# Kernel tuning notes

Hardware: AMD Instinct MI355X
Metric: run time of the kernel (lower is better)

## Reference

```python
import jax, jax.numpy as jnp
import numpy as np

N = 50000       # nodes
E = 800000      # directed edges (before self-loops)
D_IN = 128
H = 32          # hidden width, heads=1 (PyG SuperGATConv defaults)
D_OUT = 16
L = 15          # stacked SuperGATConv layers
NEG_SLOPE = 0.2


def setup_inputs() -> dict:
    key = jax.random.key(0)
    ks = jax.random.split(key, 8)
    s_in = 1.0 / np.sqrt(D_IN)
    s_h = 1.0 / np.sqrt(H)
    return dict(
        x=jax.random.normal(ks[0], (N, D_IN), jnp.float32),
        edge_index=jax.random.randint(ks[1], (2, E), 0, N, jnp.int32),
        W0=jax.random.normal(ks[2], (D_IN, H), jnp.float32) * s_in,
        b0=jnp.zeros((H,), jnp.float32),
        Ws=jax.random.normal(ks[3], (L, H, H), jnp.float32) * s_h,
        att_l=jax.random.normal(ks[4], (L, H), jnp.float32) * s_h,
        att_r=jax.random.normal(ks[5], (L, H), jnp.float32) * s_h,
        bs=jnp.zeros((L, H), jnp.float32),
        W16=jax.random.normal(ks[6], (H, D_OUT), jnp.float32) * s_h,
        b16=jnp.zeros((D_OUT,), jnp.float32),
    )


def _supergat(h, src, dst, W, al, ar, b):
    # One SuperGATConv (attention_type='MX', heads=1, concat) forward.
    hp = h @ W                          # [N, H] transformed features
    hj = hp[src]                        # [E', H] source (message) features
    hi = hp[dst]                        # [E', H] destination features
    logits = jnp.sum(hi * hj, axis=-1)  # MX dot-product logits
    alpha = hj @ al + hi @ ar           # GAT-style additive scores
    alpha = alpha * jax.nn.sigmoid(logits)
    alpha = jnp.where(alpha >= 0, alpha, NEG_SLOPE * alpha)  # leaky_relu
    # segment softmax over destination nodes
    amax = jax.ops.segment_max(alpha, dst, num_segments=N)
    ex = jnp.exp(alpha - amax[dst])
    den = jax.ops.segment_sum(ex, dst, num_segments=N)
    coef = ex / den[dst]
    out = jax.ops.segment_sum(hj * coef[:, None], dst, num_segments=N)
    return out + b


def reference(x, edge_index, W0, b0, Ws, att_l, att_r, bs, W16, b16):
    # PyG SuperGATConv adds self-loops by default
    loops = jnp.arange(N, dtype=edge_index.dtype)
    src = jnp.concatenate([edge_index[0], loops])
    dst = jnp.concatenate([edge_index[1], loops])
    h = x @ W0 + b0                     # conv0: Linear(in, 32)

    def step(h, p):
        W, al, ar, b = p
        return jax.nn.relu(_supergat(h, src, dst, W, al, ar, b)), None

    h, _ = jax.lax.scan(step, h, (Ws, att_l, att_r, bs))
    return h @ W16 + b16                # conv16: Linear(32, out)
```

## Files before the change

### kernel.cpp

```cpp
#include <hip/hip_runtime.h>
#include <hip/hip_fp16.h>
#include <cmath>
#include <cstring>

#define NN 50000
#define EE 800000
#define ET 850000
#define PADCAP 1004544
#define NBK 831
#define EBINS 196
#define DB 512
#define NB 50

__global__ void k_fill(int* __restrict__ p){
  int i = blockIdx.x*256 + threadIdx.x;
  p[i] = NN;
}

__global__ void k_permfill(int* __restrict__ perm){
  int i = blockIdx.x*256 + threadIdx.x;
  perm[i] = NN;
}

__global__ __launch_bounds__(1024) void k_ebhist(const int* __restrict__ ei,
                                                 int* __restrict__ ebh){
  __shared__ int hist[EBINS];
  int t = threadIdx.x, b = blockIdx.x;
  if (t < EBINS) hist[t] = 0;
  __syncthreads();
  int e = b*1024 + t;
  if (e < ET){
    int d = (e < EE) ? ei[EE + e] : (e - EE);
    atomicAdd(&hist[d >> 8], 1);
  }
  __syncthreads();
  if (t < EBINS) ebh[t*NBK + b] = hist[t];
}

__global__ __launch_bounds__(1024) void k_escan1(const int* __restrict__ ebh,
                                                 int* __restrict__ ebhoff,
                                                 int* __restrict__ btot){
  __shared__ int tmp[1024];
  int bin = blockIdx.x, t = threadIdx.x;
  int v = (t < NBK) ? ebh[bin*NBK + t] : 0;
  int inc = v;
  for (int off = 1; off < 1024; off <<= 1){
    tmp[t] = inc; __syncthreads();
    int add = (t >= off) ? tmp[t - off] : 0;
    __syncthreads();
    inc += add;
  }
  if (t < NBK) ebhoff[bin*NBK + t] = inc - v;
  if (t == 1023) btot[bin] = inc;
}

__global__ __launch_bounds__(256) void k_escan2(const int* __restrict__ btot,
                                                int* __restrict__ bbase){
  __shared__ int tmp[256];
  int t = threadIdx.x;
  int v = (t < EBINS) ? btot[t] : 0;
  int inc = v;
  for (int off = 1; off < 256; off <<= 1){
    tmp[t] = inc; __syncthreads();
    int add = (t >= off) ? tmp[t - off] : 0;
    __syncthreads();
    inc += add;
  }
  if (t < EBINS) bbase[t] = inc - v;
  if (t == 255) bbase[EBINS] = inc;
}

__global__ __launch_bounds__(1024) void k_ebin(const int* __restrict__ ei,
                                               const int* __restrict__ ebhoff,
                                               const int* __restrict__ bbase,
                                               int2* __restrict__ ebuf){
  __shared__ int hist[EBINS];
  int t = threadIdx.x, b = blockIdx.x;
  if (t < EBINS) hist[t] = 0;
  __syncthreads();
  int e = b*1024 + t;
  if (e < ET){
    int s, d;
    if (e < EE){ s = ei[e]; d = ei[EE + e]; } else { s = d = e - EE; }
    int bin = d >> 8;
    int rank = atomicAdd(&hist[bin], 1);
    int pos = bbase[bin] + ebhoff[bin*NBK + b] + rank;
    ebuf[pos] = make_int2(s, d);
  }
}

__global__ __launch_bounds__(1024) void k_ecnt(const int2* __restrict__ ebuf,
                                               const int* __restrict__ bbase,
                                               int* __restrict__ count){
  __shared__ int cnt[256];
  int t = threadIdx.x, bin = blockIdx.x;
  if (t < 256) cnt[t] = 0;
  __syncthreads();
  int rb = bbase[bin], re = bbase[bin+1];
  for (int i = rb + t; i < re; i += 1024) atomicAdd(&cnt[ebuf[i].y - (bin << 8)], 1);
  __syncthreads();
  int idx = (bin << 8) + t;
  if (t < 256 && idx < NN) count[idx] = cnt[t];
}

__global__ void k_bsum(const int* __restrict__ count, int* __restrict__ bsums){
  int i = blockIdx.x*256 + threadIdx.x;
  int v = (i < NN) ? ((count[i] + 3) & ~3) : 0;
  #pragma unroll
  for (int m = 1; m < 64; m <<= 1) v += __shfl_xor(v, m);
  __shared__ int ws[4];
  if ((threadIdx.x & 63) == 0) ws[threadIdx.x >> 6] = v;
  __syncthreads();
  if (threadIdx.x == 0) bsums[blockIdx.x] = ws[0] + ws[1] + ws[2] + ws[3];
}

__global__ void k_bscan(const int* __restrict__ bsums, int* __restrict__ boffs, int nb){
  __shared__ int tmp[256];
  int t = threadIdx.x;
  int self = (t < nb) ? bsums[t] : 0;
  int v = self;
  for (int off = 1; off < 256; off <<= 1){
    tmp[t] = v; __syncthreads();
    int add = (t >= off) ? tmp[t - off] : 0;
    __syncthreads();
    v += add;
  }
  if (t < nb) boffs[t] = v - self;
}

__global__ void k_scan(const int* __restrict__ count, const int* __restrict__ boffs,
                       int* __restrict__ offs){
  __shared__ int tmp[256];
  int t = threadIdx.x;
  int gid = blockIdx.x*256 + t;
  int self = (gid < NN) ? ((count[gid] + 3) & ~3) : 0;
  int v = self;
  for (int off = 1; off < 256; off <<= 1){
    tmp[t] = v; __syncthreads();
    int add = (t >= off) ? tmp[t - off] : 0;
    __syncthreads();
    v += add;
  }
  int excl = v - self + boffs[blockIdx.x];
  if (gid < NN) offs[gid] = excl;
  if (gid == NN-1) offs[NN] = excl + self;
}

__global__ __launch_bounds__(1024) void k_escatter(const int2* __restrict__ ebuf,
                                                   const int* __restrict__ bbase,
                                                   const int* __restrict__ offs,
                                                   int* __restrict__ srcCSR){
  __shared__ int cur[256];
  int t = threadIdx.x, bin = blockIdx.x;
  if (t < 256){ int idx = (bin << 8) + t; cur[t] = (idx < NN) ? offs[idx] : 0; }
  __syncthreads();
  int rb = bbase[bin], re = bbase[bin+1];
  for (int i = rb + t; i < re; i += 1024){
    int2 e = ebuf[i];
    int p = atomicAdd(&cur[e.y - (bin << 8)], 1);
    srcCSR[p] = e.x;
  }
}

__global__ __launch_bounds__(1024) void k_dhist_blk(const int* __restrict__ count,
                                                    int* __restrict__ blockhist){
  __shared__ int hist[DB];
  int t = threadIdx.x, b = blockIdx.x;
  if (t < DB) hist[t] = 0;
  __syncthreads();
  int i = b*1024 + t;
  if (i < NN){
    int deg = count[i]; if (deg > DB-1) deg = DB-1;
    atomicAdd(&hist[DB-1-deg], 1);
  }
  __syncthreads();
  if (t < DB) blockhist[t*NB + b] = hist[t];
}

__global__ __launch_bounds__(DB) void k_dcol(const int* __restrict__ blockhist,
                                             int* __restrict__ blockoffs,
                                             int* __restrict__ dbase){
  int k = threadIdx.x;
  int run = 0;
  #pragma unroll 5
  for (int b = 0; b < NB; ++b){
    int v = blockhist[k*NB + b];
    blockoffs[k*NB + b] = run;
    run += v;
  }
  __shared__ int tmp[DB];
  int v = run;
  for (int off = 1; off < DB; off <<= 1){
    tmp[k] = v; __syncthreads();
    int add = (k >= off) ? tmp[k - off] : 0;
    __syncthreads();
    v += add;
  }
  dbase[k] = v - run;
}

__global__ __launch_bounds__(1024) void k_dscatter_blk(const int* __restrict__ count,
                                                       const int* __restrict__ blockoffs,
                                                       const int* __restrict__ dbase,
                                                       int* __restrict__ perm){
  __shared__ int hist[DB];
  int t = threadIdx.x, b = blockIdx.x;
  if (t < DB) hist[t] = 0;
  __syncthreads();
  int i = b*1024 + t;
  if (i < NN){
    int deg = count[i]; if (deg > DB-1) deg = DB-1;
    int bin = DB-1-deg;
    int rank = atomicAdd(&hist[bin], 1);
    int pos = dbase[bin] + blockoffs[bin*NB + b] + rank;
    perm[pos] = i;
  }
}

__device__ __forceinline__ void cvt8(uint4 r, float* v){
  __half2 h;
  memcpy(&h, &r.x, 4); float2 f = __half22float2(h); v[0]=f.x; v[1]=f.y;
  memcpy(&h, &r.y, 4); f = __half22float2(h); v[2]=f.x; v[3]=f.y;
  memcpy(&h, &r.z, 4); f = __half22float2(h); v[4]=f.x; v[5]=f.y;
  memcpy(&h, &r.w, 4); f = __half22float2(h); v[6]=f.x; v[7]=f.y;
}
__device__ __forceinline__ unsigned pack_h2(float x, float y){
  __half2 h = __floats2half2_rn(x, y);
  unsigned u; memcpy(&u, &h, 4); return u;
}

__global__ __launch_bounds__(256) void k_prologue(
    const float* __restrict__ x, const float* __restrict__ W0, const float* __restrict__ b0,
    const float* __restrict__ Ws0, const float* __restrict__ al0, const float* __restrict__ ar0,
    __half* __restrict__ hp_out, float* __restrict__ hl_out, float* __restrict__ hr_out){
  __shared__ __align__(16) float w0[128*32];
  __shared__ __align__(16) float w1[32*32];
  int t = threadIdx.x;
  for (int i = t; i < 4096; i += 256) w0[i] = W0[i];
  for (int i = t; i < 1024; i += 256) w1[i] = Ws0[i];
  __syncthreads();
  int g = t >> 5, lane = t & 31;
  float bl = b0[lane], alv = al0[lane], arv = ar0[lane];
  #pragma unroll
  for (int p = 0; p < 2; ++p){
    int na = blockIdx.x*32 + p*16 + g;
    int nb = na + 8;
    int nac = (na < NN) ? na : NN-1;
    int nbc = (nb < NN) ? nb : NN-1;
    const float4* xa = (const float4*)(x + (size_t)nac*128);
    const float4* xb4 = (const float4*)(x + (size_t)nbc*128);
    float ha = bl, hb = bl;
    #pragma unroll
    for (int j4 = 0; j4 < 32; ++j4){
      float4 va = xa[j4], vb = xb4[j4];
      float c0 = w0[(j4*4+0)*32 + lane], c1 = w0[(j4*4+1)*32 + lane];
      float c2 = w0[(j4*4+2)*32 + lane], c3 = w0[(j4*4+3)*32 + lane];
      ha += va.x*c0 + va.y*c1 + va.z*c2 + va.w*c3;
      hb += vb.x*c0 + vb.y*c1 + vb.z*c2 + vb.w*c3;
    }
    float hpa = 0.f, hpb = 0.f;
    #pragma unroll
    for (int j = 0; j < 32; ++j){
      float w = w1[j*32 + lane];
      hpa += __shfl(ha, j, 32) * w;
      hpb += __shfl(hb, j, 32) * w;
    }
    float tla = hpa*alv, tra = hpa*arv, tlb = hpb*alv, trb = hpb*arv;
    #pragma unroll
    for (int m = 1; m < 32; m <<= 1){
      tla += __shfl_xor(tla, m); tra += __shfl_xor(tra, m);
      tlb += __shfl_xor(tlb, m); trb += __shfl_xor(trb, m);
    }
    if (na < NN){
      hp_out[(size_t)na*32 + lane] = __float2half(hpa);
      if (lane == 0){ hl_out[na] = tla; hr_out[na] = tra; }
    }
    if (nb < NN){
      hp_out[(size_t)nb*32 + lane] = __float2half(hpb);
      if (lane == 0){ hl_out[nb] = tlb; hr_out[nb] = trb; }
    }
  }
  if (blockIdx.x == 0){
    if (t < 32) hp_out[(size_t)NN*32 + t] = __float2half(0.f);
    if (t == 0) hl_out[NN] = -1e30f;
  }
}

__global__ __launch_bounds__(256) void k_layer(
    const __half* __restrict__ hp, const float* __restrict__ hl, const float* __restrict__ hr,
    const int* __restrict__ offs, const int* __restrict__ srcCSR, const int* __restrict__ perm,
    const float* __restrict__ bcur,
    const float* __restrict__ Wn, const float* __restrict__ aln, const float* __restrict__ arn,
    const float* __restrict__ b16,
    __half* __restrict__ hp_out, float* __restrict__ hl_out, float* __restrict__ hr_out,
    float* __restrict__ final_out, int last){
  __shared__ __align__(16) float wl[1024];
  __shared__ __align__(16) float xb[64*36];
  int t = threadIdx.x;
  int nW = last ? 512 : 1024;
  for (int i = t; i < nW; i += 256) wl[i] = Wn[i];
  int lane = t & 63;
  int li = lane & 3;
  int slot = t >> 2;
  int d = perm[blockIdx.x*64 + slot];
  int beg = offs[d];
  int lenP = offs[d+1] - beg;
  int ng = (d < NN) ? (lenP >> 2) : 0;
  float hpd[8];
  cvt8(*(const uint4*)(hp + ((size_t)d << 5) + (li << 3)), hpd);
  float hrd = hr[d];

  int maxg = ng;
  #pragma unroll
  for (int m = 1; m < 64; m <<= 1) maxg = max(maxg, __shfl_xor(maxg, m));

  auto LD4 = [&](int g)->int4{
    int4 q = *(const int4*)(srcCSR + beg + (g << 2));
    if (g >= ng){ q.x = NN; q.y = NN; q.z = NN; q.w = NN; }
    return q;
  };
  auto ROW = [&](int s)->uint4{
    return *(const uint4*)(hp + ((size_t)s << 5) + (li << 3));
  };
  float acc[8] = {0.f,0.f,0.f,0.f,0.f,0.f,0.f,0.f};
  float den = 0.f;
  auto EDGE = [&](uint4 r, float gl){
    float v[8];
    cvt8(r, v);
    float p = v[0]*hpd[0] + v[1]*hpd[1] + v[2]*hpd[2] + v[3]*hpd[3]
            + v[4]*hpd[4] + v[5]*hpd[5] + v[6]*hpd[6] + v[7]*hpd[7];
    p += __shfl_xor(p, 1); p += __shfl_xor(p, 2);
    float a = (gl + hrd) * (1.f/(1.f + __expf(-p)));
    a = fmaxf(a, 0.2f*a);
    float e = __expf(a);
    den += e;
    #pragma unroll
    for (int k = 0; k < 8; ++k) acc[k] += v[k]*e;
  };

  int4 qA = LD4(0);
  uint4 rA0=ROW(qA.x), rA1=ROW(qA.y), rA2=ROW(qA.z), rA3=ROW(qA.w);
  float gA0=hl[qA.x], gA1=hl[qA.y], gA2=hl[qA.z], gA3=hl[qA.w];
  int4 qB = LD4(1);

  for (int g = 0; g < maxg; g += 2){
    uint4 rB0=ROW(qB.x), rB1=ROW(qB.y), rB2=ROW(qB.z), rB3=ROW(qB.w);
    float gB0=hl[qB.x], gB1=hl[qB.y], gB2=hl[qB.z], gB3=hl[qB.w];
    int4 qN = LD4(g + 2);
    EDGE(rA0,gA0); EDGE(rA1,gA1); EDGE(rA2,gA2); EDGE(rA3,gA3);
    rA0=ROW(qN.x); rA1=ROW(qN.y); rA2=ROW(qN.z); rA3=ROW(qN.w);
    gA0=hl[qN.x]; gA1=hl[qN.y]; gA2=hl[qN.z]; gA3=hl[qN.w];
    qB = LD4(g + 3);
    EDGE(rB0,gB0); EDGE(rB1,gB1); EDGE(rB2,gB2); EDGE(rB3,gB3);
  }

  float rden = 1.f/den;
  const float4* bc4 = (const float4*)bcur;
  float4 ba = bc4[2*li], bb = bc4[2*li+1];
  float* hrow = xb + slot*36;
  {
    float4 h0, h1;
    h0.x = fmaxf(acc[0]*rden + ba.x, 0.f);
    h0.y = fmaxf(acc[1]*rden + ba.y, 0.f);
    h0.z = fmaxf(acc[2]*rden + ba.z, 0.f);
    h0.w = fmaxf(acc[3]*rden + ba.w, 0.f);
    h1.x = fmaxf(acc[4]*rden + bb.x, 0.f);
    h1.y = fmaxf(acc[5]*rden + bb.y, 0.f);
    h1.z = fmaxf(acc[6]*rden + bb.z, 0.f);
    h1.w = fmaxf(acc[7]*rden + bb.w, 0.f);
    *((float4*)hrow + 2*li) = h0;
    *((float4*)hrow + 2*li + 1) = h1;
  }
  __syncthreads();

  const float4* wl4 = (const float4*)wl;
  if (!last){
    float o[8] = {0.f,0.f,0.f,0.f,0.f,0.f,0.f,0.f};
    #pragma unroll
    for (int k = 0; k < 32; ++k){
      float hk = hrow[k];
      float4 wa = wl4[k*8 + 2*li];
      float4 wb = wl4[k*8 + 2*li + 1];
      o[0]+=hk*wa.x; o[1]+=hk*wa.y; o[2]+=hk*wa.z; o[3]+=hk*wa.w;
      o[4]+=hk*wb.x; o[5]+=hk*wb.y; o[6]+=hk*wb.z; o[7]+=hk*wb.w;
    }
    const float4* a4 = (const float4*)aln;
    const float4* r4 = (const float4*)arn;
    float4 aa = a4[2*li], ab = a4[2*li+1];
    float4 ra = r4[2*li], rb = r4[2*li+1];
    float tl = o[0]*aa.x+o[1]*aa.y+o[2]*aa.z+o[3]*aa.w
             + o[4]*ab.x+o[5]*ab.y+o[6]*ab.z+o[7]*ab.w;
    float tr = o[0]*ra.x+o[1]*ra.y+o[2]*ra.z+o[3]*ra.w
             + o[4]*rb.x+o[5]*rb.y+o[6]*rb.z+o[7]*rb.w;
    tl += __shfl_xor(tl, 1); tl += __shfl_xor(tl, 2);
    tr += __shfl_xor(tr, 1); tr += __shfl_xor(tr, 2);
    if (d < NN){
      uint4 st;
      st.x = pack_h2(o[0], o[1]); st.y = pack_h2(o[2], o[3]);
      st.z = pack_h2(o[4], o[5]); st.w = pack_h2(o[6], o[7]);
      *(uint4*)(hp_out + ((size_t)d << 5) + (li << 3)) = st;
      if (li == 0){ hl_out[d] = tl; hr_out[d] = tr; }
    }
    if (blockIdx.x == 0){
      if (t < 32) hp_out[(size_t)NN*32 + t] = __float2half(0.f);
      if (t == 0) hl_out[NN] = -1e30f;
    }
  } else {
    float4 o = ((const float4*)b16)[li];
    #pragma unroll
    for (int k = 0; k < 32; ++k){
      float hk = hrow[k];
      float4 wv = wl4[k*4 + li];
      o.x += hk*wv.x; o.y += hk*wv.y; o.z += hk*wv.z; o.w += hk*wv.w;
    }
    if (d < NN) *((float4*)(final_out + (size_t)d*16) + li) = o;
  }
}

extern "C" void kernel_launch(void* const* d_in, const int* in_sizes, int n_in,
                              void* d_out, int out_size, void* d_ws, size_t ws_size,
                              hipStream_t stream){
  const float* x   = (const float*)d_in[0];
  const int*   ei  = (const int*)  d_in[1];
  const float* W0  = (const float*)d_in[2];
  const float* b0  = (const float*)d_in[3];
  const float* Ws  = (const float*)d_in[4];
  const float* al  = (const float*)d_in[5];
  const float* ar  = (const float*)d_in[6];
  const float* bs  = (const float*)d_in[7];
  const float* W16 = (const float*)d_in[8];
  const float* b16 = (const float*)d_in[9];
  float* out = (float*)d_out;

  char* w = (char*)d_ws;
  int* count     = (int*)w;   w += 50176*sizeof(int);
  int* offs      = (int*)w;   w += 50432*sizeof(int);
  int* srcCSR    = (int*)w;   w += (size_t)PADCAP*sizeof(int);
  int* bsums     = (int*)w;   w += 256*sizeof(int);
  int* boffs     = (int*)w;   w += 256*sizeof(int);
  int* perm      = (int*)w;   w += 50176*sizeof(int);
  int* blockhist = (int*)w;   w += DB*NB*sizeof(int);
  int* blockoffs = (int*)w;   w += DB*NB*sizeof(int);
  int* dbase     = (int*)w;   w += DB*sizeof(int);
  int* ebh       = (int*)w;   w += (size_t)EBINS*NBK*sizeof(int) + 16;
  int* ebhoff    = (int*)w;   w += (size_t)EBINS*NBK*sizeof(int) + 16;
  int* btot      = (int*)w;   w += 256*sizeof(int);
  int* bbase     = (int*)w;   w += 256*sizeof(int);
  int2* ebuf     = (int2*)w;  w += (size_t)(NBK*1024)*sizeof(int2);
  __half* hpA  = (__half*)w; w += (size_t)(NN+16)*32*sizeof(__half);
  __half* hpB  = (__half*)w; w += (size_t)(NN+16)*32*sizeof(__half);
  float* hlA   = (float*)w; w += 50176*sizeof(float);
  float* hrA   = (float*)w; w += 50176*sizeof(float);
  float* hlB   = (float*)w; w += 50176*sizeof(float);
  float* hrB   = (float*)w; w += 50176*sizeof(float);

  k_fill    <<<PADCAP/256, 256, 0, stream>>>(srcCSR);
  k_permfill<<<196, 256, 0, stream>>>(perm);
  k_ebhist  <<<NBK, 1024, 0, stream>>>(ei, ebh);
  k_escan1  <<<EBINS, 1024, 0, stream>>>(ebh, ebhoff, btot);
  k_escan2  <<<1, 256, 0, stream>>>(btot, bbase);
  k_ebin    <<<NBK, 1024, 0, stream>>>(ei, ebhoff, bbase, ebuf);
  k_ecnt    <<<EBINS, 1024, 0, stream>>>(ebuf, bbase, count);
  k_bsum    <<<196, 256, 0, stream>>>(count, bsums);
  k_bscan   <<<1, 256, 0, stream>>>(bsums, boffs, 196);
  k_scan    <<<196, 256, 0, stream>>>(count, boffs, offs);
  k_escatter<<<EBINS, 1024, 0, stream>>>(ebuf, bbase, offs, srcCSR);
  k_dhist_blk   <<<NB, 1024, 0, stream>>>(count, blockhist);
  k_dcol        <<<1,  DB,   0, stream>>>(blockhist, blockoffs, dbase);
  k_dscatter_blk<<<NB, 1024, 0, stream>>>(count, blockoffs, dbase, perm);

  k_prologue<<<1563, 256, 0, stream>>>(x, W0, b0, Ws, al, ar, hpA, hlA, hrA);

  int nblk = (50048) / 64;
  for (int l = 0; l < 15; ++l){
    const __half* hin = (l & 1) ? hpB : hpA;
    const float* hlin = (l & 1) ? hlB : hlA;
    const float* hrin = (l & 1) ? hrB : hrA;
    __half* hout = (l & 1) ? hpA : hpB;
    float* hlout = (l & 1) ? hlA : hlB;
    float* hrout = (l & 1) ? hrA : hrB;
    int last = (l == 14);
    const float* Wn  = last ? W16 : (Ws + (size_t)(l+1)*1024);
    const float* aln = last ? al  : (al + (size_t)(l+1)*32);
    const float* arn = last ? ar  : (ar + (size_t)(l+1)*32);
    k_layer<<<nblk, 256, 0, stream>>>(hin, hlin, hrin, offs, srcCSR, perm,
                                      bs + (size_t)l*32,
                                      Wn, aln, arn, b16,
                                      hout, hlout, hrout, out, last);
  }
}
```

Baseline: 497.4 us.

## Compute attention scores in-kernel from gathered rows; retile prologue through shared memory

The per-node attention projections hl/hr are no longer precomputed and stored. Each edge now computes the source-side score as a dot of the gathered fp16 row with att_l, and the destination score is computed once per node. This removes the scattered hl gathers and the hl/hr writes in exchange for extra FMAs and shuffles per edge, and padded edges are masked explicitly. The prologue is also rewritten to stage x transposed in shared memory, with 8 threads per node computing float4 outputs.

```diff
diff --git a/kernel.cpp b/kernel.cpp
--- a/kernel.cpp
+++ b/kernel.cpp
@@ -231,69 +231,67 @@
 
 __global__ __launch_bounds__(256) void k_prologue(
     const float* __restrict__ x, const float* __restrict__ W0, const float* __restrict__ b0,
-    const float* __restrict__ Ws0, const float* __restrict__ al0, const float* __restrict__ ar0,
-    __half* __restrict__ hp_out, float* __restrict__ hl_out, float* __restrict__ hr_out){
-  __shared__ __align__(16) float w0[128*32];
-  __shared__ __align__(16) float w1[32*32];
-  int t = threadIdx.x;
-  for (int i = t; i < 4096; i += 256) w0[i] = W0[i];
-  for (int i = t; i < 1024; i += 256) w1[i] = Ws0[i];
-  __syncthreads();
-  int g = t >> 5, lane = t & 31;
-  float bl = b0[lane], alv = al0[lane], arv = ar0[lane];
+    const float* __restrict__ Ws0, __half* __restrict__ hp_out){
+  __shared__ __align__(16) float xs[128*33];
+  __shared__ __align__(16) float w0s[128*32];
+  __shared__ __align__(16) float w1s[32*32];
+  int t = threadIdx.x, b = blockIdx.x;
   #pragma unroll
-  for (int p = 0; p < 2; ++p){
-    int na = blockIdx.x*32 + p*16 + g;
-    int nb = na + 8;
-    int nac = (na < NN) ? na : NN-1;
-    int nbc = (nb < NN) ? nb : NN-1;
-    const float4* xa = (const float4*)(x + (size_t)nac*128);
-    const float4* xb4 = (const float4*)(x + (size_t)nbc*128);
-    float ha = bl, hb = bl;
+  for (int k = 0; k < 4; ++k){
+    int i = t + k*256;
+    int n = i >> 5, j4 = (i & 31) << 2;
+    int r = b*32 + n;
+    const float4* src = (const float4*)(x + (size_t)((r < NN) ? r : 0)*128);
+    float4 v = src[i & 31];
+    xs[(j4+0)*33 + n] = v.x;
+    xs[(j4+1)*33 + n] = v.y;
+    xs[(j4+2)*33 + n] = v.z;
+    xs[(j4+3)*33 + n] = v.w;
+  }
+  {
+    const float4* w04 = (const float4*)W0;
+    float4* dst = (float4*)w0s;
     #pragma unroll
-    for (int j4 = 0; j4 < 32; ++j4){
-      float4 va = xa[j4], vb = xb4[j4];
-      float c0 = w0[(j4*4+0)*32 + lane], c1 = w0[(j4*4+1)*32 + lane];
-      float c2 = w0[(j4*4+2)*32 + lane], c3 = w0[(j4*4+3)*32 + lane];
-      ha += va.x*c0 + va.y*c1 + va.z*c2 + va.w*c3;
-      hb += vb.x*c0 + vb.y*c1 + vb.z*c2 + vb.w*c3;
-    }
-    float hpa = 0.f, hpb = 0.f;
-    #pragma unroll
-    for (int j = 0; j < 32; ++j){
-      float w = w1[j*32 + lane];
-      hpa += __shfl(ha, j, 32) * w;
-      hpb += __shfl(hb, j, 32) * w;
-    }
-    float tla = hpa*alv, tra = hpa*arv, tlb = hpb*alv, trb = hpb*arv;
-    #pragma unroll
-    for (int m = 1; m < 32; m <<= 1){
-      tla += __shfl_xor(tla, m); tra += __shfl_xor(tra, m);
-      tlb += __shfl_xor(tlb, m); trb += __shfl_xor(trb, m);
-    }
-    if (na < NN){
-      hp_out[(size_t)na*32 + lane] = __float2half(hpa);
-      if (lane == 0){ hl_out[na] = tla; hr_out[na] = tra; }
-    }
-    if (nb < NN){
-      hp_out[(size_t)nb*32 + lane] = __float2half(hpb);
-      if (lane == 0){ hl_out[nb] = tlb; hr_out[nb] = trb; }
-    }
-  }
-  if (blockIdx.x == 0){
-    if (t < 32) hp_out[(size_t)NN*32 + t] = __float2half(0.f);
-    if (t == 0) hl_out[NN] = -1e30f;
-  }
+    for (int k = 0; k < 4; ++k) dst[t + k*256] = w04[t + k*256];
+    ((float4*)w1s)[t] = ((const float4*)Ws0)[t];
+  }
+  __syncthreads();
+  int nloc = t >> 3, c8 = t & 7;
+  float4 acc = ((const float4*)b0)[c8];
+  const float* xcol = xs + nloc;
+  const float4* w0r = (const float4*)w0s + c8;
+  #pragma unroll 8
+  for (int j = 0; j < 128; ++j){
+    float xv = xcol[j*33];
+    float4 wv = w0r[j*8];
+    acc.x += xv*wv.x; acc.y += xv*wv.y; acc.z += xv*wv.z; acc.w += xv*wv.w;
+  }
+  __syncthreads();
+  float* hs = w0s;
+  ((float4*)(hs + nloc*36))[c8] = acc;
+  float4 o = {0.f,0.f,0.f,0.f};
+  const float* hrow = hs + nloc*36;
+  const float4* w1r = (const float4*)w1s + c8;
+  #pragma unroll 8
+  for (int j = 0; j < 32; ++j){
+    float hv = hrow[j];
+    float4 wv = w1r[j*8];
+    o.x += hv*wv.x; o.y += hv*wv.y; o.z += hv*wv.z; o.w += hv*wv.w;
+  }
+  int n = b*32 + nloc;
+  if (n < NN){
+    uint2 st; st.x = pack_h2(o.x, o.y); st.y = pack_h2(o.z, o.w);
+    *(uint2*)(hp_out + (size_t)n*32 + (c8 << 2)) = st;
+  }
+  if (b == 0 && t < 32) hp_out[(size_t)NN*32 + t] = __float2half(0.f);
 }
 
 __global__ __launch_bounds__(256) void k_layer(
-    const __half* __restrict__ hp, const float* __restrict__ hl, const float* __restrict__ hr,
+    const __half* __restrict__ hp,
     const int* __restrict__ offs, const int* __restrict__ srcCSR, const int* __restrict__ perm,
-    const float* __restrict__ bcur,
-    const float* __restrict__ Wn, const float* __restrict__ aln, const float* __restrict__ arn,
-    const float* __restrict__ b16,
-    __half* __restrict__ hp_out, float* __restrict__ hl_out, float* __restrict__ hr_out,
-    float* __restrict__ final_out, int last){
+    const float* __restrict__ bcur, const float* __restrict__ alc, const float* __restrict__ arc,
+    const float* __restrict__ Wn, const float* __restrict__ b16,
+    __half* __restrict__ hp_out, float* __restrict__ final_out, int last){
   __shared__ __align__(16) float wl[1024];
   __shared__ __align__(16) float xb[64*36];
   int t = threadIdx.x;
@@ -308,7 +306,11 @@
   int ng = (d < NN) ? (lenP >> 2) : 0;
   float hpd[8];
   cvt8(*(const uint4*)(hp + ((size_t)d << 5) + (li << 3)), hpd);
-  float hrd = hr[d];
+  float4 ala = ((const float4*)alc)[2*li], alb = ((const float4*)alc)[2*li+1];
+  float4 ara = ((const float4*)arc)[2*li], arb = ((const float4*)arc)[2*li+1];
+  float hrd = hpd[0]*ara.x + hpd[1]*ara.y + hpd[2]*ara.z + hpd[3]*ara.w
+            + hpd[4]*arb.x + hpd[5]*arb.y + hpd[6]*arb.z + hpd[7]*arb.w;
+  hrd += __shfl_xor(hrd, 1); hrd += __shfl_xor(hrd, 2);
 
   int maxg = ng;
   #pragma unroll
@@ -324,15 +326,19 @@
   };
   float acc[8] = {0.f,0.f,0.f,0.f,0.f,0.f,0.f,0.f};
   float den = 0.f;
-  auto EDGE = [&](uint4 r, float gl){
+  auto EDGE = [&](uint4 r, int s){
     float v[8];
     cvt8(r, v);
     float p = v[0]*hpd[0] + v[1]*hpd[1] + v[2]*hpd[2] + v[3]*hpd[3]
             + v[4]*hpd[4] + v[5]*hpd[5] + v[6]*hpd[6] + v[7]*hpd[7];
+    float q = v[0]*ala.x + v[1]*ala.y + v[2]*ala.z + v[3]*ala.w
+            + v[4]*alb.x + v[5]*alb.y + v[6]*alb.z + v[7]*alb.w;
     p += __shfl_xor(p, 1); p += __shfl_xor(p, 2);
-    float a = (gl + hrd) * (1.f/(1.f + __expf(-p)));
+    q += __shfl_xor(q, 1); q += __shfl_xor(q, 2);
+    float a = (q + hrd) * (1.f/(1.f + __expf(-p)));
     a = fmaxf(a, 0.2f*a);
     float e = __expf(a);
+    e = (s < NN) ? e : 0.f;
     den += e;
     #pragma unroll
     for (int k = 0; k < 8; ++k) acc[k] += v[k]*e;
@@ -340,18 +346,17 @@
 
   int4 qA = LD4(0);
   uint4 rA0=ROW(qA.x), rA1=ROW(qA.y), rA2=ROW(qA.z), rA3=ROW(qA.w);
-  float gA0=hl[qA.x], gA1=hl[qA.y], gA2=hl[qA.z], gA3=hl[qA.w];
   int4 qB = LD4(1);
 
   for (int g = 0; g < maxg; g += 2){
     uint4 rB0=ROW(qB.x), rB1=ROW(qB.y), rB2=ROW(qB.z), rB3=ROW(qB.w);
-    float gB0=hl[qB.x], gB1=hl[qB.y], gB2=hl[qB.z], gB3=hl[qB.w];
     int4 qN = LD4(g + 2);
-    EDGE(rA0,gA0); EDGE(rA1,gA1); EDGE(rA2,gA2); EDGE(rA3,gA3);
+    EDGE(rA0,qA.x); EDGE(rA1,qA.y); EDGE(rA2,qA.z); EDGE(rA3,qA.w);
     rA0=ROW(qN.x); rA1=ROW(qN.y); rA2=ROW(qN.z); rA3=ROW(qN.w);
-    gA0=hl[qN.x]; gA1=hl[qN.y]; gA2=hl[qN.z]; gA3=hl[qN.w];
-    qB = LD4(g + 3);
-    EDGE(rB0,gB0); EDGE(rB1,gB1); EDGE(rB2,gB2); EDGE(rB3,gB3);
+    qA = qN;
+    int4 qB2 = LD4(g + 3);
+    EDGE(rB0,qB.x); EDGE(rB1,qB.y); EDGE(rB2,qB.z); EDGE(rB3,qB.w);
+    qB = qB2;
   }
 
   float rden = 1.f/den;
@@ -384,26 +389,14 @@
       o[0]+=hk*wa.x; o[1]+=hk*wa.y; o[2]+=hk*wa.z; o[3]+=hk*wa.w;
       o[4]+=hk*wb.x; o[5]+=hk*wb.y; o[6]+=hk*wb.z; o[7]+=hk*wb.w;
     }
-    const float4* a4 = (const float4*)aln;
-    const float4* r4 = (const float4*)arn;
-    float4 aa = a4[2*li], ab = a4[2*li+1];
-    float4 ra = r4[2*li], rb = r4[2*li+1];
-    float tl = o[0]*aa.x+o[1]*aa.y+o[2]*aa.z+o[3]*aa.w
-             + o[4]*ab.x+o[5]*ab.y+o[6]*ab.z+o[7]*ab.w;
-    float tr = o[0]*ra.x+o[1]*ra.y+o[2]*ra.z+o[3]*ra.w
-             + o[4]*rb.x+o[5]*rb.y+o[6]*rb.z+o[7]*rb.w;
-    tl += __shfl_xor(tl, 1); tl += __shfl_xor(tl, 2);
-    tr += __shfl_xor(tr, 1); tr += __shfl_xor(tr, 2);
     if (d < NN){
       uint4 st;
       st.x = pack_h2(o[0], o[1]); st.y = pack_h2(o[2], o[3]);
       st.z = pack_h2(o[4], o[5]); st.w = pack_h2(o[6], o[7]);
       *(uint4*)(hp_out + ((size_t)d << 5) + (li << 3)) = st;
-      if (li == 0){ hl_out[d] = tl; hr_out[d] = tr; }
     }
     if (blockIdx.x == 0){
       if (t < 32) hp_out[(size_t)NN*32 + t] = __float2half(0.f);
-      if (t == 0) hl_out[NN] = -1e30f;
     }
   } else {
     float4 o = ((const float4*)b16)[li];
@@ -449,10 +442,6 @@
   int2* ebuf     = (int2*)w;  w += (size_t)(NBK*1024)*sizeof(int2);
   __half* hpA  = (__half*)w; w += (size_t)(NN+16)*32*sizeof(__half);
   __half* hpB  = (__half*)w; w += (size_t)(NN+16)*32*sizeof(__half);
-  float* hlA   = (float*)w; w += 50176*sizeof(float);
-  float* hrA   = (float*)w; w += 50176*sizeof(float);
-  float* hlB   = (float*)w; w += 50176*sizeof(float);
-  float* hrB   = (float*)w; w += 50176*sizeof(float);
 
   k_fill    <<<PADCAP/256, 256, 0, stream>>>(srcCSR);
   k_permfill<<<196, 256, 0, stream>>>(perm);
@@ -469,23 +458,18 @@
   k_dcol        <<<1,  DB,   0, stream>>>(blockhist, blockoffs, dbase);
   k_dscatter_blk<<<NB, 1024, 0, stream>>>(count, blockoffs, dbase, perm);
 
-  k_prologue<<<1563, 256, 0, stream>>>(x, W0, b0, Ws, al, ar, hpA, hlA, hrA);
-
-  int nblk = (50048) / 64;
+  k_prologue<<<1563, 256, 0, stream>>>(x, W0, b0, Ws, hpA);
+
+  int nblk = 50048 / 64;
   for (int l = 0; l < 15; ++l){
     const __half* hin = (l & 1) ? hpB : hpA;
-    const float* hlin = (l & 1) ? hlB : hlA;
-    const float* hrin = (l & 1) ? hrB : hrA;
     __half* hout = (l & 1) ? hpA : hpB;
-    float* hlout = (l & 1) ? hlA : hlB;
-    float* hrout = (l & 1) ? hrA : hrB;
     int last = (l == 14);
     const float* Wn  = last ? W16 : (Ws + (size_t)(l+1)*1024);
-    const float* aln = last ? al  : (al + (size_t)(l+1)*32);
-    const float* arn = last ? ar  : (ar + (size_t)(l+1)*32);
-    k_layer<<<nblk, 256, 0, stream>>>(hin, hlin, hrin, offs, srcCSR, perm,
+    k_layer<<<nblk, 256, 0, stream>>>(hin, offs, srcCSR, perm,
                                       bs + (size_t)l*32,
-                                      Wn, aln, arn, b16,
-                                      hout, hlout, hrout, out, last);
-  }
-}
+                                      al + (size_t)l*32, ar + (size_t)l*32,
+                                      Wn, b16,
+                                      hout, out, last);
+  }
+}
```

After: 436.3 us. -12.3%, faster.
